# Kernel tuning notes

Hardware: AMD Instinct MI355X
Metric: run time of the kernel (lower is better)

Reference implementation:

```python
import jax, jax.numpy as jnp
import numpy as np

B, P, CV = 2, 1024, 768
V, DNB, K = 50000, 300, 3
H = 768  # max(512, v_dim)
TOTAL_IN = CV + K * DNB + K  # include_scores=True
EPS = 1e-12


def setup_inputs() -> dict:
    key = jax.random.key(0)
    ks = jax.random.split(key, 7)
    v_seq = jax.random.normal(ks[0], (B, P, CV), dtype=jnp.float32)
    T = jax.random.normal(ks[1], (V, CV), dtype=jnp.float32)
    T_clip = T / jnp.linalg.norm(T, axis=-1, keepdims=True)  # bank rows are L2-normalized
    nb_vecs = jax.random.normal(ks[2], (V, DNB), dtype=jnp.float32)
    W1 = jax.random.normal(ks[3], (TOTAL_IN, H), dtype=jnp.float32) * (1.0 / np.sqrt(TOTAL_IN))
    b1 = jnp.zeros((H,), dtype=jnp.float32)
    W2 = jax.random.normal(ks[4], (H, CV), dtype=jnp.float32) * (1.0 / np.sqrt(H))
    b2 = jnp.zeros((CV,), dtype=jnp.float32)
    return {"v_seq": v_seq, "T_clip": T_clip, "nb_vecs": nb_vecs,
            "W1": W1, "b1": b1, "W2": W2, "b2": b2}


def _layer_norm(x, eps=1e-5):
    mu = jnp.mean(x, axis=-1, keepdims=True)
    var = jnp.var(x, axis=-1, keepdims=True)
    return (x - mu) * jax.lax.rsqrt(var + eps)


def reference(v_seq, T_clip, nb_vecs, W1, b1, W2, b2):
    # --- retrieve (no_grad in original) ---
    q = v_seq / jnp.maximum(jnp.linalg.norm(v_seq, axis=-1, keepdims=True), EPS)
    S = jnp.einsum('bpc,vc->bpv', q, T_clip)            # (B,P,V) cosine sims
    val, idx = jax.lax.top_k(S, K)                       # (B,P,K) each
    nb_sel = nb_vecs[idx]                                # gather -> (B,P,K,DNB)
    # --- fuse_concat ---
    nb_flat = nb_sel.reshape(B, P, K * DNB)
    combined = jnp.concatenate([v_seq, nb_flat, val], axis=-1)  # (B,P,TOTAL_IN)
    h = jax.nn.gelu(combined @ W1 + b1, approximate=False)      # nn.GELU default = erf
    fused = h @ W2 + b2                                          # dropout inactive (eval)
    return _layer_norm(fused)                                    # F.layer_norm, no affine
```

## Files before the change

### kernel.cpp

```cpp
#include <hip/hip_runtime.h>
#include <hip/hip_bf16.h>

typedef unsigned short u16;
typedef unsigned int u32;
typedef __attribute__((ext_vector_type(4))) unsigned short u16x4;
typedef __attribute__((ext_vector_type(8))) unsigned short u16x8;
typedef __attribute__((ext_vector_type(8))) short bf16x8;
typedef __attribute__((ext_vector_type(4))) float f32x4;

#define ROWS 2048
#define CV 768
#define VOCAB 50000
#define NPAD 50176
#define NTILES 196
#define NSEG 392
#define NSEGP 392
#define DNB 300
#define TOTAL_IN 1671
#define KPAD1 1696
#define HD 768
#define NT 12
#define CVT_BLOCKS 2048
#define W1T_BLOCKS (53 * 24)
#define W2T_BLOCKS (24 * 24)

__device__ __forceinline__ u16 f2bf(float f) {
  union { __hip_bfloat16 h; u16 u; } x;
  x.h = __float2bfloat16(f);
  return x.u;
}

__device__ __forceinline__ u16 bfkey(u16 u) {
  return (u & 0x8000) ? (u16)~u : (u16)(u | 0x8000);
}

__device__ __forceinline__ void gload16(const u16* g, const u16* l) {
  __builtin_amdgcn_global_load_lds(
      (const __attribute__((address_space(1))) void*)g,
      (__attribute__((address_space(3))) void*)l, 16, 0, 0);
}

__device__ __forceinline__ float block_sum256(float v, float* ws) {
#pragma unroll
  for (int off = 32; off > 0; off >>= 1) v += __shfl_xor(v, off, 64);
  int tid = threadIdx.x;
  if ((tid & 63) == 0) ws[tid >> 6] = v;
  __syncthreads();
  float s = ws[0] + ws[1] + ws[2] + ws[3];
  __syncthreads();
  return s;
}

__device__ __forceinline__ void transpose_tile(
    const float* __restrict__ src, u16* __restrict__ dst,
    int Ksrc, int ldk, int N, int kb, int nb, float (*tile)[33]) {
  int tx = threadIdx.x & 31, ty = threadIdx.x >> 5;
#pragma unroll
  for (int i = 0; i < 4; ++i) {
    int k = kb + ty + i * 8, n = nb + tx;
    tile[ty + i * 8][tx] = (k < Ksrc) ? src[(size_t)k * N + n] : 0.f;
  }
  __syncthreads();
#pragma unroll
  for (int i = 0; i < 4; ++i) {
    int n = nb + ty + i * 8, k = kb + tx;
    dst[(size_t)n * ldk + k] = f2bf(tile[tx][ty + i * 8]);
  }
}

__global__ __launch_bounds__(256) void prep_kernel(
    const float* __restrict__ v_seq, float* __restrict__ rinv, u16* __restrict__ q16,
    const float* __restrict__ T, u16* __restrict__ T16,
    const float* __restrict__ W1, u16* __restrict__ W1T,
    const float* __restrict__ W2, u16* __restrict__ W2T) {
  __shared__ float tile[32][33];
  int b = blockIdx.x, tid = threadIdx.x;
  if (b < ROWS) {
    float* ws = &tile[0][0];
    const float* x = v_seq + (size_t)b * CV;
    float x0 = x[tid], x1 = x[tid + 256], x2 = x[tid + 512];
    float s = block_sum256(x0 * x0 + x1 * x1 + x2 * x2, ws);
    float denom = fmaxf(sqrtf(s), 1e-12f);
    float inv = 1.0f / denom;
    u16* qb = q16 + (size_t)b * CV;
    qb[tid] = f2bf(x0 * inv); qb[tid + 256] = f2bf(x1 * inv); qb[tid + 512] = f2bf(x2 * inv);
    if (tid == 0) rinv[b] = inv;
  } else if (b < ROWS + CVT_BLOCKS) {
    int i = (b - ROWS) * 256 + tid;
    const int n4 = VOCAB * CV / 4;
    const int stride = CVT_BLOCKS * 256;
    for (; i < n4; i += stride) {
      float4 v = reinterpret_cast<const float4*>(T)[i];
      u16x4 o = {f2bf(v.x), f2bf(v.y), f2bf(v.z), f2bf(v.w)};
      reinterpret_cast<u16x4*>(T16)[i] = o;
    }
  } else if (b < ROWS + CVT_BLOCKS + W1T_BLOCKS) {
    int bb = b - ROWS - CVT_BLOCKS;
    transpose_tile(W1, W1T, TOTAL_IN, KPAD1, HD, (bb % 53) * 32, (bb / 53) * 32, tile);
  } else {
    int bb = b - ROWS - CVT_BLOCKS - W1T_BLOCKS;
    transpose_tile(W2, W2T, HD, HD, HD, (bb % 24) * 32, (bb / 24) * 32, tile);
  }
}

__global__ __launch_bounds__(512, 2) void score_gemm_256(
    const u16* __restrict__ q16, const u16* __restrict__ T16,
    u16* __restrict__ S16, u16* __restrict__ segmax) {
  __shared__ __align__(16) u16 lds[65536];
  __shared__ float smx[256][4];

  int tid = threadIdx.x;
  int w = tid >> 6, lane = tid & 63;
  int wr = w >> 2, wc = w & 3;
  int l15 = lane & 15, l4 = lane >> 4;

  int bid = blockIdx.x;
  int wg = (bid & 7) * NTILES + (bid >> 3);
  int mtile = wg & 7, ntile = wg >> 3;
  int m0 = mtile * 256, n0 = ntile * 256;

  int t8 = tid >> 3;
  int jcol = (((tid & 7) ^ (t8 & 7)) << 3);
  int rowA = m0 + t8;
  int rowB0 = n0 + t8;        rowB0 = rowB0 > (VOCAB - 1) ? (VOCAB - 1) : rowB0;
  int rowB1 = n0 + 64 + t8;   rowB1 = rowB1 > (VOCAB - 1) ? (VOCAB - 1) : rowB1;
  int rowB2 = n0 + 128 + t8;  rowB2 = rowB2 > (VOCAB - 1) ? (VOCAB - 1) : rowB2;
  int rowB3 = n0 + 192 + t8;  rowB3 = rowB3 > (VOCAB - 1) ? (VOCAB - 1) : rowB3;
  int w512 = w * 512;

  int xorv = (l15 & 7) << 4;
  int l416 = l4 << 4;
  int c0 = ((l416) ^ xorv) >> 1;
  int c1 = ((64 + l416) ^ xorv) >> 1;
  int aro = (wr * 128 + l15) * 64;
  int bro = 16384 + (wc * 64 + l15) * 64;

  f32x4 acc[8][4];
#pragma unroll
  for (int i = 0; i < 8; ++i)
#pragma unroll
    for (int j = 0; j < 4; ++j) acc[i][j] = {0.f, 0.f, 0.f, 0.f};

  bf16x8 af[2][4], bfr[2][4];

#define STAGE_A(R0) gload16(q16 + (size_t)(rowA + (R0)) * CV + ktn + jcol, \
                            &lds[nbase + (R0) * 64 + w512])
#define STAGE_B0() gload16(T16 + (size_t)rowB0 * CV + ktn + jcol, &lds[nbase + 16384 + w512])
#define STAGE_B1() gload16(T16 + (size_t)rowB1 * CV + ktn + jcol, &lds[nbase + 16384 + 4096 + w512])
#define STAGE_B2() gload16(T16 + (size_t)rowB2 * CV + ktn + jcol, &lds[nbase + 16384 + 8192 + w512])
#define STAGE_B3() gload16(T16 + (size_t)rowB3 * CV + ktn + jcol, &lds[nbase + 16384 + 12288 + w512])

#define LDA4(MIB)                                                           \
  _Pragma("unroll") for (int ks = 0; ks < 2; ++ks)                          \
  _Pragma("unroll") for (int mi = 0; mi < 4; ++mi)                          \
    af[ks][mi] = *reinterpret_cast<const bf16x8*>(                          \
        &lds[cbase + aro + ((MIB) + mi) * 1024 + (ks ? c1 : c0)]);

#define LDB2(NIB)                                                           \
  _Pragma("unroll") for (int ks = 0; ks < 2; ++ks)                          \
  _Pragma("unroll") for (int ni = 0; ni < 2; ++ni)                          \
    bfr[ks][(NIB) + ni] = *reinterpret_cast<const bf16x8*>(                 \
        &lds[cbase + bro + ((NIB) + ni) * 1024 + (ks ? c1 : c0)]);

#define MFMAQ(MIB, NIB)                                                     \
  _Pragma("unroll") for (int mi = 0; mi < 4; ++mi)                          \
  _Pragma("unroll") for (int ni = 0; ni < 2; ++ni) {                        \
    acc[(MIB) + mi][(NIB) + ni] = __builtin_amdgcn_mfma_f32_16x16x32_bf16(  \
        af[0][mi], bfr[0][(NIB) + ni], acc[(MIB) + mi][(NIB) + ni], 0, 0, 0); \
    acc[(MIB) + mi][(NIB) + ni] = __builtin_amdgcn_mfma_f32_16x16x32_bf16(  \
        af[1][mi], bfr[1][(NIB) + ni], acc[(MIB) + mi][(NIB) + ni], 0, 0, 0); \
  }

  {
    int nbase = 0, ktn = 0;
    STAGE_B0(); STAGE_B1(); STAGE_B2(); STAGE_B3();
    STAGE_A(0); STAGE_A(128); STAGE_A(64); STAGE_A(192);
  }

  for (int t = 0; t < NT; ++t) {
    int cb = t & 1;
    int cbase = cb * 32768;
    int nbase = cbase ^ 32768;
    int ktn = ((t + 1 < NT) ? (t + 1) : t) * 64;

    asm volatile("s_waitcnt vmcnt(2)" ::: "memory");
    __builtin_amdgcn_s_barrier();
    __builtin_amdgcn_sched_barrier(0);

    LDA4(0)
    LDB2(0)
    STAGE_B0(); STAGE_B1();
    __builtin_amdgcn_s_setprio(1);
    MFMAQ(0, 0)
    __builtin_amdgcn_s_setprio(0);

    LDB2(2)
    STAGE_B2(); STAGE_B3();
    __builtin_amdgcn_s_setprio(1);
    MFMAQ(0, 2)
    __builtin_amdgcn_s_setprio(0);

    asm volatile("s_waitcnt vmcnt(4)" ::: "memory");
    __builtin_amdgcn_s_barrier();
    __builtin_amdgcn_sched_barrier(0);

    LDA4(4)
    STAGE_A(0); STAGE_A(128);
    __builtin_amdgcn_s_setprio(1);
    MFMAQ(4, 0)
    __builtin_amdgcn_s_setprio(0);

    STAGE_A(64); STAGE_A(192);
    __builtin_amdgcn_s_setprio(1);
    MFMAQ(4, 2)
    __builtin_amdgcn_s_setprio(0);
  }
  asm volatile("s_waitcnt vmcnt(0)" ::: "memory");
  asm volatile("s_waitcnt lgkmcnt(0)" ::: "memory");
  __syncthreads();

#pragma unroll
  for (int mi = 0; mi < 8; ++mi)
#pragma unroll
    for (int ni = 0; ni < 4; ++ni) {
      int gr = m0 + wr * 128 + mi * 16 + l4 * 4;
      int gc = n0 + wc * 64 + ni * 16 + l15;
#pragma unroll
      for (int r = 0; r < 4; ++r)
        S16[(size_t)(gr + r) * NPAD + gc] = f2bf(acc[mi][ni][r]);
    }

#pragma unroll
  for (int mi = 0; mi < 8; ++mi)
#pragma unroll
    for (int r = 0; r < 4; ++r) {
      float v = -3e38f;
#pragma unroll
      for (int ni = 0; ni < 4; ++ni) {
        bool ok = (n0 + wc * 64 + ni * 16 + l15) < VOCAB;
        v = fmaxf(v, ok ? acc[mi][ni][r] : -3e38f);
      }
#pragma unroll
      for (int d = 1; d < 16; d <<= 1) v = fmaxf(v, __shfl_xor(v, d, 64));
      if (l15 == 0) smx[wr * 128 + mi * 16 + l4 * 4 + r][wc] = v;
    }
  __syncthreads();
  if (tid < 256) {
    float s0 = fmaxf(smx[tid][0], smx[tid][1]);
    float s1 = fmaxf(smx[tid][2], smx[tid][3]);
    segmax[(size_t)(m0 + tid) * NSEGP + 2 * ntile]     = bfkey(f2bf(s0));
    segmax[(size_t)(m0 + tid) * NSEGP + 2 * ntile + 1] = bfkey(f2bf(s1));
  }
#undef STAGE_A
#undef STAGE_B0
#undef STAGE_B1
#undef STAGE_B2
#undef STAGE_B3
#undef LDA4
#undef LDB2
#undef MFMAQ
}

template <int ACT, int OUTBF>
__global__ __launch_bounds__(256) void gemm_bt64(
    const u16* __restrict__ A, int lda,
    const u16* __restrict__ B, int ldb, int nclamp,
    int Kdim, const float* __restrict__ bias,
    float* __restrict__ Cf, u16* __restrict__ Cb, int ldc) {
  __shared__ __align__(16) u16 Asm[64 * 32];
  __shared__ __align__(16) u16 Bsm[128 * 32];
  int tid = threadIdx.x;
  int w = tid >> 6, lane = tid & 63;
  int wr = w >> 1, wc = w & 1;
  int m0 = blockIdx.x * 64;
  int n0 = blockIdx.y * 128;
  f32x4 acc[2][4];
#pragma unroll
  for (int i = 0; i < 2; ++i)
#pragma unroll
    for (int j = 0; j < 4; ++j) acc[i][j] = {0.f, 0.f, 0.f, 0.f};

  int r0 = tid >> 2, s0 = tid & 3;
  int b0r = n0 + r0;       b0r = b0r > nclamp ? nclamp : b0r;
  int b1r = n0 + 64 + r0;  b1r = b1r > nclamp ? nclamp : b1r;

  for (int k0 = 0; k0 < Kdim; k0 += 32) {
    __syncthreads();
    gload16(A + (size_t)(m0 + r0) * lda + k0 + s0 * 8, Asm + w * 512);
    gload16(B + (size_t)b0r * ldb + k0 + s0 * 8, Bsm + w * 512);
    gload16(B + (size_t)b1r * ldb + k0 + s0 * 8, Bsm + 2048 + w * 512);
    __syncthreads();
    int l15 = lane & 15, l4 = lane >> 4;
    bf16x8 af[2], bfr[4];
#pragma unroll
    for (int mi = 0; mi < 2; ++mi)
      af[mi] = *reinterpret_cast<const bf16x8*>(Asm + (wr * 32 + mi * 16 + l15) * 32 + l4 * 8);
#pragma unroll
    for (int ni = 0; ni < 4; ++ni)
      bfr[ni] = *reinterpret_cast<const bf16x8*>(Bsm + (wc * 64 + ni * 16 + l15) * 32 + l4 * 8);
#pragma unroll
    for (int mi = 0; mi < 2; ++mi)
#pragma unroll
      for (int ni = 0; ni < 4; ++ni)
        acc[mi][ni] = __builtin_amdgcn_mfma_f32_16x16x32_bf16(af[mi], bfr[ni], acc[mi][ni], 0, 0, 0);
  }

  int l15 = lane & 15, l4 = lane >> 4;
#pragma unroll
  for (int mi = 0; mi < 2; ++mi) {
#pragma unroll
    for (int ni = 0; ni < 4; ++ni) {
      int gr = m0 + wr * 32 + mi * 16 + l4 * 4;
      int gc = n0 + wc * 64 + ni * 16 + l15;
      float bv = bias ? bias[gc] : 0.f;
#pragma unroll
      for (int r = 0; r < 4; ++r) {
        float x = acc[mi][ni][r] + bv;
        if (ACT) x = 0.5f * x * (1.0f + erff(x * 0.70710678118654752f));
        size_t co = (size_t)(gr + r) * ldc + gc;
        if (OUTBF) Cb[co] = f2bf(x);
        else       Cf[co] = x;
      }
    }
  }
}

__global__ __launch_bounds__(256) void select_kernel(
    const u16* __restrict__ segmax, const u16* __restrict__ S,
    const float* __restrict__ v_seq, const float* __restrict__ rinv,
    const float* __restrict__ T, const float* __restrict__ nb,
    u16* __restrict__ c16) {
  __shared__ u32 skey[448];
  __shared__ u32 winners[16];
  __shared__ u32 cl[256][16];
  __shared__ int scand[16];
  __shared__ float sex[16];
  __shared__ float sval[3];
  __shared__ int sidx[3];
  int row = blockIdx.x, tid = threadIdx.x;

  if (tid < 224) {
#pragma unroll
    for (int j = 0; j < 2; ++j) {
      int s = tid * 2 + j;
      u32 k = 0;
      if (s < NSEG) k = ((u32)segmax[(size_t)row * NSEGP + s] << 9) | (u32)(511 - s);
      skey[s] = k;
    }
  }
  __syncthreads();

  if (tid < 64) {
    u32 v[7];
#pragma unroll
    for (int j = 0; j < 7; ++j) v[j] = skey[tid + 64 * j];
#pragma unroll
    for (int rd = 0; rd < 16; ++rd) {
      u32 m = v[0];
#pragma unroll
      for (int j = 1; j < 7; ++j) m = (v[j] > m) ? v[j] : m;
#pragma unroll
      for (int d = 1; d < 64; d <<= 1) {
        u32 o = (u32)__shfl_xor((int)m, d, 64);
        m = (o > m) ? o : m;
      }
#pragma unroll
      for (int j = 0; j < 7; ++j) v[j] = (v[j] == m) ? 0u : v[j];
      if (tid == 0) winners[rd] = m;
    }
  }
  __syncthreads();

  int wi = tid >> 4, off = (tid & 15) * 8;
  int seg = 511 - (int)(winners[wi] & 511);
  const u16* Sr = S + (size_t)row * NPAD + seg * 128 + off;
  u16x8 vv = *reinterpret_cast<const u16x8*>(Sr);
  u32 ck[8];
  int gbase = seg * 128 + off;
#pragma unroll
  for (int jj = 0; jj < 8; ++jj) {
    int g = gbase + jj;
    u32 c = ((u32)bfkey(vv[jj]) << 16) | (u32)(0xFFFF - g);
    ck[jj] = (g >= VOCAB) ? 0u : c;
  }
#define CE(i, j) { u32 a = ck[i], b = ck[j]; ck[i] = a > b ? a : b; ck[j] = a > b ? b : a; }
  CE(0,1) CE(2,3) CE(4,5) CE(6,7)
  CE(0,2) CE(1,3) CE(4,6) CE(5,7)
  CE(1,2) CE(5,6)
  CE(0,4) CE(1,5) CE(2,6) CE(3,7)
  CE(2,4) CE(3,5)
  CE(1,2) CE(3,4) CE(5,6)
#undef CE
#pragma unroll
  for (int k = 0; k < 8; ++k) cl[tid][k] = ck[k];
#pragma unroll
  for (int k = 8; k < 16; ++k) cl[tid][k] = 0u;
  __syncthreads();

  for (int s = 128; s >= 1; s >>= 1) {
    if (tid < s) {
      u32 ov[16];
      int pa = 0, pb = 0;
#pragma unroll
      for (int k = 0; k < 16; ++k) {
        u32 va = cl[tid][pa], vb = cl[tid + s][pb];
        bool ta = va >= vb;
        ov[k] = ta ? va : vb;
        pa += ta ? 1 : 0;
        pb += ta ? 0 : 1;
      }
#pragma unroll
      for (int k = 0; k < 16; ++k) cl[tid][k] = ov[k];
    }
    __syncthreads();
  }
  if (tid < 16) scand[tid] = 0xFFFF - (int)(cl[0][tid] & 0xFFFF);
  __syncthreads();

  int wv = tid >> 6, lane = tid & 63;
  const float* __restrict__ qr = v_seq + (size_t)row * CV;
  float ri = rinv[row];
#pragma unroll
  for (int c0 = 0; c0 < 4; ++c0) {
    int c = wv + c0 * 4;
    int n = scand[c];
    const float* tr = T + (size_t)n * CV;
    float part = 0.f;
    int kb = lane * 12;
#pragma unroll
    for (int j3 = 0; j3 < 3; ++j3) {
      float4 a = *reinterpret_cast<const float4*>(tr + kb + j3 * 4);
      float4 b = *reinterpret_cast<const float4*>(qr + kb + j3 * 4);
      part += a.x * b.x + a.y * b.y + a.z * b.z + a.w * b.w;
    }
#pragma unroll
    for (int off2 = 32; off2 >= 1; off2 >>= 1) part += __shfl_xor(part, off2, 64);
    if (lane == 0) sex[c] = part * ri;
  }
  __syncthreads();
  if (tid == 0) {
    float xv[16]; int xi[16];
#pragma unroll
    for (int c = 0; c < 16; ++c) { xv[c] = sex[c]; xi[c] = scand[c]; }
    for (int t = 0; t < 3; ++t) {
      float bv = -__builtin_inff(); int bi = 0x7fffffff, bc = -1;
#pragma unroll
      for (int c = 0; c < 16; ++c) {
        if (xi[c] < 0) continue;
        if (xv[c] > bv || (xv[c] == bv && xi[c] < bi)) { bv = xv[c]; bi = xi[c]; bc = c; }
      }
      sval[t] = bv; sidx[t] = bi;
      xi[bc] = -1;
    }
  }
  __syncthreads();

  u16* c = c16 + (size_t)row * KPAD1;
  if (tid < 192) {
    float4 v = *reinterpret_cast<const float4*>(qr + tid * 4);
    u16x4 o = {f2bf(v.x), f2bf(v.y), f2bf(v.z), f2bf(v.w)};
    *reinterpret_cast<u16x4*>(c + tid * 4) = o;
  }
  int i0 = sidx[0], i1 = sidx[1], i2 = sidx[2];
  if (tid < 75) {
    float4 v = *reinterpret_cast<const float4*>(nb + (size_t)i0 * DNB + tid * 4);
    u16x4 o = {f2bf(v.x), f2bf(v.y), f2bf(v.z), f2bf(v.w)};
    *reinterpret_cast<u16x4*>(c + CV + tid * 4) = o;
    v = *reinterpret_cast<const float4*>(nb + (size_t)i1 * DNB + tid * 4);
    o = {f2bf(v.x), f2bf(v.y), f2bf(v.z), f2bf(v.w)};
    *reinterpret_cast<u16x4*>(c + CV + DNB + tid * 4) = o;
    v = *reinterpret_cast<const float4*>(nb + (size_t)i2 * DNB + tid * 4);
    o = {f2bf(v.x), f2bf(v.y), f2bf(v.z), f2bf(v.w)};
    *reinterpret_cast<u16x4*>(c + CV + 2 * DNB + tid * 4) = o;
  }
  if (tid < 28) {
    int o = CV + 3 * DNB + tid;
    c[o] = (tid < 3) ? f2bf(sval[tid]) : (u16)0;
  }
}

__global__ __launch_bounds__(256) void layernorm_kernel(float* __restrict__ C) {
  __shared__ float ws[4];
  int row = blockIdx.x, tid = threadIdx.x;
  float* x = C + (size_t)row * CV;
  float x0 = x[tid], x1 = x[tid + 256], x2 = x[tid + 512];
  float mu = block_sum256(x0 + x1 + x2, ws) * (1.0f / 768.0f);
  float d0 = x0 - mu, d1 = x1 - mu, d2 = x2 - mu;
  float var = block_sum256(d0 * d0 + d1 * d1 + d2 * d2, ws) * (1.0f / 768.0f);
  float inv = 1.0f / sqrtf(var + 1e-5f);
  x[tid] = d0 * inv; x[tid + 256] = d1 * inv; x[tid + 512] = d2 * inv;
}

extern "C" void kernel_launch(void* const* d_in, const int* in_sizes, int n_in,
                              void* d_out, int out_size, void* d_ws, size_t ws_size,
                              hipStream_t stream) {
  const float* v_seq = (const float*)d_in[0];
  const float* T = (const float*)d_in[1];
  const float* nb = (const float*)d_in[2];
  const float* W1 = (const float*)d_in[3];
  const float* b1 = (const float*)d_in[4];
  const float* W2 = (const float*)d_in[5];
  const float* b2 = (const float*)d_in[6];
  float* out = (float*)d_out;

  char* base = (char*)d_ws;
  size_t off = 0;
  auto alloc = [&](size_t bytes) -> void* {
    void* p = base + off;
    off += (bytes + 255) & ~(size_t)255;
    return p;
  };
  float* rinv = (float*)alloc((size_t)ROWS * 4);
  u16* q16   = (u16*)alloc((size_t)ROWS * CV * 2);
  u16* T16   = (u16*)alloc((size_t)VOCAB * CV * 2);
  u16* c16   = (u16*)alloc((size_t)ROWS * KPAD1 * 2);
  u16* h16   = (u16*)alloc((size_t)ROWS * HD * 2);
  u16* W1T   = (u16*)alloc((size_t)HD * KPAD1 * 2);
  u16* W2T   = (u16*)alloc((size_t)HD * HD * 2);
  u16* segmaxb = (u16*)alloc((size_t)ROWS * NSEGP * 2);
  u16* S16   = (u16*)alloc((size_t)ROWS * NPAD * 2);

  prep_kernel<<<ROWS + CVT_BLOCKS + W1T_BLOCKS + W2T_BLOCKS, 256, 0, stream>>>(
      v_seq, rinv, q16, T, T16, W1, W1T, W2, W2T);
  score_gemm_256<<<8 * NTILES, 512, 0, stream>>>(q16, T16, S16, segmaxb);
  select_kernel<<<ROWS, 256, 0, stream>>>(segmaxb, S16, v_seq, rinv, T, nb, c16);
  gemm_bt64<1, 1><<<dim3(ROWS / 64, HD / 128), 256, 0, stream>>>(
      c16, KPAD1, W1T, KPAD1, HD - 1, KPAD1, b1, nullptr, h16, HD);
  gemm_bt64<0, 0><<<dim3(ROWS / 64, HD / 128), 256, 0, stream>>>(
      h16, HD, W2T, HD, HD - 1, HD, b2, out, nullptr, HD);
  layernorm_kernel<<<ROWS, 256, 0, stream>>>(out);
}
```

Measured before the change: 396.7 us.

## Shrink score GEMM tile to 256x128 with BK=32 for higher occupancy

Replaces the 256x256, BK=64 score GEMM with a 256x128, BK=32 tile, giving each wave a 64x64 sub-tile and a smaller double-buffered LDS footprint. Launch bounds move from 2 to 4 blocks per CU, and the tile count doubles so each tile writes one segment max instead of two. The aim is better latency hiding and more even CU balance. The cost is lower arithmetic intensity per tile, so the vocab matrix is re-read less efficiently and twice as many barriers run per K step.

```diff
diff --git a/kernel.cpp b/kernel.cpp
--- a/kernel.cpp
+++ b/kernel.cpp
@@ -12,14 +12,14 @@
 #define CV 768
 #define VOCAB 50000
 #define NPAD 50176
-#define NTILES 196
+#define NTILES 392
 #define NSEG 392
 #define NSEGP 392
 #define DNB 300
 #define TOTAL_IN 1671
 #define KPAD1 1696
 #define HD 768
-#define NT 12
+#define NT2 24
 #define CVT_BLOCKS 2048
 #define W1T_BLOCKS (53 * 24)
 #define W2T_BLOCKS (24 * 24)
@@ -103,116 +103,80 @@
   }
 }
 
-__global__ __launch_bounds__(512, 2) void score_gemm_256(
+__global__ __launch_bounds__(512, 4) void score_gemm_bk32(
     const u16* __restrict__ q16, const u16* __restrict__ T16,
     u16* __restrict__ S16, u16* __restrict__ segmax) {
-  __shared__ __align__(16) u16 lds[65536];
-  __shared__ float smx[256][4];
+  __shared__ __align__(16) u16 lds[24576];
+  __shared__ float smx[256][2];
 
   int tid = threadIdx.x;
   int w = tid >> 6, lane = tid & 63;
-  int wr = w >> 2, wc = w & 3;
+  int wr = w >> 1, wc = w & 1;
   int l15 = lane & 15, l4 = lane >> 4;
 
   int bid = blockIdx.x;
   int wg = (bid & 7) * NTILES + (bid >> 3);
   int mtile = wg & 7, ntile = wg >> 3;
-  int m0 = mtile * 256, n0 = ntile * 256;
-
-  int t8 = tid >> 3;
-  int jcol = (((tid & 7) ^ (t8 & 7)) << 3);
-  int rowA = m0 + t8;
-  int rowB0 = n0 + t8;        rowB0 = rowB0 > (VOCAB - 1) ? (VOCAB - 1) : rowB0;
-  int rowB1 = n0 + 64 + t8;   rowB1 = rowB1 > (VOCAB - 1) ? (VOCAB - 1) : rowB1;
-  int rowB2 = n0 + 128 + t8;  rowB2 = rowB2 > (VOCAB - 1) ? (VOCAB - 1) : rowB2;
-  int rowB3 = n0 + 192 + t8;  rowB3 = rowB3 > (VOCAB - 1) ? (VOCAB - 1) : rowB3;
-  int w512 = w * 512;
-
-  int xorv = (l15 & 7) << 4;
-  int l416 = l4 << 4;
-  int c0 = ((l416) ^ xorv) >> 1;
-  int c1 = ((64 + l416) ^ xorv) >> 1;
-  int aro = (wr * 128 + l15) * 64;
-  int bro = 16384 + (wc * 64 + l15) * 64;
-
-  f32x4 acc[8][4];
-#pragma unroll
-  for (int i = 0; i < 8; ++i)
+  int m0 = mtile * 256, n0 = ntile * 128;
+
+  int t4 = tid >> 2;
+  int jcol = (((tid & 3) ^ (t4 & 3)) << 3);
+  int tid8 = tid * 8;
+  const u16* pA0 = q16 + (size_t)(m0 + t4) * CV + jcol;
+  const u16* pA1 = q16 + (size_t)(m0 + 128 + t4) * CV + jcol;
+  int rowB = n0 + t4; rowB = rowB > (VOCAB - 1) ? (VOCAB - 1) : rowB;
+  const u16* pB = T16 + (size_t)rowB * CV + jcol;
+
+  int coff = ((l4 ^ (l15 & 3)) << 3);
+  int aro = (wr * 64 + l15) * 32;
+  int bro = 8192 + (wc * 64 + l15) * 32;
+
+  f32x4 acc[4][4];
+#pragma unroll
+  for (int i = 0; i < 4; ++i)
 #pragma unroll
     for (int j = 0; j < 4; ++j) acc[i][j] = {0.f, 0.f, 0.f, 0.f};
 
-  bf16x8 af[2][4], bfr[2][4];
-
-#define STAGE_A(R0) gload16(q16 + (size_t)(rowA + (R0)) * CV + ktn + jcol, \
-                            &lds[nbase + (R0) * 64 + w512])
-#define STAGE_B0() gload16(T16 + (size_t)rowB0 * CV + ktn + jcol, &lds[nbase + 16384 + w512])
-#define STAGE_B1() gload16(T16 + (size_t)rowB1 * CV + ktn + jcol, &lds[nbase + 16384 + 4096 + w512])
-#define STAGE_B2() gload16(T16 + (size_t)rowB2 * CV + ktn + jcol, &lds[nbase + 16384 + 8192 + w512])
-#define STAGE_B3() gload16(T16 + (size_t)rowB3 * CV + ktn + jcol, &lds[nbase + 16384 + 12288 + w512])
-
-#define LDA4(MIB)                                                           \
-  _Pragma("unroll") for (int ks = 0; ks < 2; ++ks)                          \
-  _Pragma("unroll") for (int mi = 0; mi < 4; ++mi)                          \
-    af[ks][mi] = *reinterpret_cast<const bf16x8*>(                          \
-        &lds[cbase + aro + ((MIB) + mi) * 1024 + (ks ? c1 : c0)]);
-
-#define LDB2(NIB)                                                           \
-  _Pragma("unroll") for (int ks = 0; ks < 2; ++ks)                          \
-  _Pragma("unroll") for (int ni = 0; ni < 2; ++ni)                          \
-    bfr[ks][(NIB) + ni] = *reinterpret_cast<const bf16x8*>(                 \
-        &lds[cbase + bro + ((NIB) + ni) * 1024 + (ks ? c1 : c0)]);
-
-#define MFMAQ(MIB, NIB)                                                     \
-  _Pragma("unroll") for (int mi = 0; mi < 4; ++mi)                          \
-  _Pragma("unroll") for (int ni = 0; ni < 2; ++ni) {                        \
-    acc[(MIB) + mi][(NIB) + ni] = __builtin_amdgcn_mfma_f32_16x16x32_bf16(  \
-        af[0][mi], bfr[0][(NIB) + ni], acc[(MIB) + mi][(NIB) + ni], 0, 0, 0); \
-    acc[(MIB) + mi][(NIB) + ni] = __builtin_amdgcn_mfma_f32_16x16x32_bf16(  \
-        af[1][mi], bfr[1][(NIB) + ni], acc[(MIB) + mi][(NIB) + ni], 0, 0, 0); \
-  }
+  bf16x8 af[4], bfr[4];
+
+#define STAGE_A0() gload16(pA0 + ktn, &lds[nbase + tid8])
+#define STAGE_A1() gload16(pA1 + ktn, &lds[nbase + 4096 + tid8])
+#define STAGE_B()  gload16(pB + ktn, &lds[nbase + 8192 + tid8])
 
   {
     int nbase = 0, ktn = 0;
-    STAGE_B0(); STAGE_B1(); STAGE_B2(); STAGE_B3();
-    STAGE_A(0); STAGE_A(128); STAGE_A(64); STAGE_A(192);
-  }
-
-  for (int t = 0; t < NT; ++t) {
-    int cb = t & 1;
-    int cbase = cb * 32768;
-    int nbase = cbase ^ 32768;
-    int ktn = ((t + 1 < NT) ? (t + 1) : t) * 64;
+    STAGE_A0(); STAGE_A1(); STAGE_B();
+  }
+
+  for (int t = 0; t < NT2; ++t) {
+    int cbase = (t & 1) * 12288;
+    int nbase = cbase ^ 12288;
+    int ktn = ((t + 1 < NT2) ? (t + 1) : t) * 32;
+
+    asm volatile("s_waitcnt vmcnt(1)" ::: "memory");
+    __builtin_amdgcn_s_barrier();
+    __builtin_amdgcn_sched_barrier(0);
+
+#pragma unroll
+    for (int mi = 0; mi < 4; ++mi)
+      af[mi] = *reinterpret_cast<const bf16x8*>(&lds[cbase + aro + mi * 512 + coff]);
+    STAGE_A0(); STAGE_A1();
 
     asm volatile("s_waitcnt vmcnt(2)" ::: "memory");
     __builtin_amdgcn_s_barrier();
     __builtin_amdgcn_sched_barrier(0);
 
-    LDA4(0)
-    LDB2(0)
-    STAGE_B0(); STAGE_B1();
+#pragma unroll
+    for (int ni = 0; ni < 4; ++ni)
+      bfr[ni] = *reinterpret_cast<const bf16x8*>(&lds[cbase + bro + ni * 512 + coff]);
+    STAGE_B();
+
     __builtin_amdgcn_s_setprio(1);
-    MFMAQ(0, 0)
-    __builtin_amdgcn_s_setprio(0);
-
-    LDB2(2)
-    STAGE_B2(); STAGE_B3();
-    __builtin_amdgcn_s_setprio(1);
-    MFMAQ(0, 2)
-    __builtin_amdgcn_s_setprio(0);
-
-    asm volatile("s_waitcnt vmcnt(4)" ::: "memory");
-    __builtin_amdgcn_s_barrier();
-    __builtin_amdgcn_sched_barrier(0);
-
-    LDA4(4)
-    STAGE_A(0); STAGE_A(128);
-    __builtin_amdgcn_s_setprio(1);
-    MFMAQ(4, 0)
-    __builtin_amdgcn_s_setprio(0);
-
-    STAGE_A(64); STAGE_A(192);
-    __builtin_amdgcn_s_setprio(1);
-    MFMAQ(4, 2)
+#pragma unroll
+    for (int mi = 0; mi < 4; ++mi)
+#pragma unroll
+      for (int ni = 0; ni < 4; ++ni)
+        acc[mi][ni] = __builtin_amdgcn_mfma_f32_16x16x32_bf16(af[mi], bfr[ni], acc[mi][ni], 0, 0, 0);
     __builtin_amdgcn_s_setprio(0);
   }
   asm volatile("s_waitcnt vmcnt(0)" ::: "memory");
@@ -220,10 +184,10 @@
   __syncthreads();
 
 #pragma unroll
-  for (int mi = 0; mi < 8; ++mi)
+  for (int mi = 0; mi < 4; ++mi)
 #pragma unroll
     for (int ni = 0; ni < 4; ++ni) {
-      int gr = m0 + wr * 128 + mi * 16 + l4 * 4;
+      int gr = m0 + wr * 64 + mi * 16 + l4 * 4;
       int gc = n0 + wc * 64 + ni * 16 + l15;
 #pragma unroll
       for (int r = 0; r < 4; ++r)
@@ -231,7 +195,7 @@
     }
 
 #pragma unroll
-  for (int mi = 0; mi < 8; ++mi)
+  for (int mi = 0; mi < 4; ++mi)
 #pragma unroll
     for (int r = 0; r < 4; ++r) {
       float v = -3e38f;
@@ -242,23 +206,16 @@
       }
 #pragma unroll
       for (int d = 1; d < 16; d <<= 1) v = fmaxf(v, __shfl_xor(v, d, 64));
-      if (l15 == 0) smx[wr * 128 + mi * 16 + l4 * 4 + r][wc] = v;
+      if (l15 == 0) smx[wr * 64 + mi * 16 + l4 * 4 + r][wc] = v;
     }
   __syncthreads();
   if (tid < 256) {
     float s0 = fmaxf(smx[tid][0], smx[tid][1]);
-    float s1 = fmaxf(smx[tid][2], smx[tid][3]);
-    segmax[(size_t)(m0 + tid) * NSEGP + 2 * ntile]     = bfkey(f2bf(s0));
-    segmax[(size_t)(m0 + tid) * NSEGP + 2 * ntile + 1] = bfkey(f2bf(s1));
-  }
-#undef STAGE_A
-#undef STAGE_B0
-#undef STAGE_B1
-#undef STAGE_B2
-#undef STAGE_B3
-#undef LDA4
-#undef LDB2
-#undef MFMAQ
+    segmax[(size_t)(m0 + tid) * NSEGP + ntile] = bfkey(f2bf(s0));
+  }
+#undef STAGE_A0
+#undef STAGE_A1
+#undef STAGE_B
 }
 
 template <int ACT, int OUTBF>
@@ -522,7 +479,7 @@
 
   prep_kernel<<<ROWS + CVT_BLOCKS + W1T_BLOCKS + W2T_BLOCKS, 256, 0, stream>>>(
       v_seq, rinv, q16, T, T16, W1, W1T, W2, W2T);
-  score_gemm_256<<<8 * NTILES, 512, 0, stream>>>(q16, T16, S16, segmaxb);
+  score_gemm_bk32<<<8 * NTILES, 512, 0, stream>>>(q16, T16, S16, segmaxb);
   select_kernel<<<ROWS, 256, 0, stream>>>(segmaxb, S16, v_seq, rinv, T, nb, c16);
   gemm_bt64<1, 1><<<dim3(ROWS / 64, HD / 128), 256, 0, stream>>>(
       c16, KPAD1, W1T, KPAD1, HD - 1, KPAD1, b1, nullptr, h16, HD);
```

Result: faster. 368.0 us (-7.2%).
